# Performance work log

Measured on AMD Instinct MI355X. Metric: run time of the kernel, lower is better.

Reference implementation:

```python
import jax, jax.numpy as jnp
import numpy as np

BATCH, NUM_MASKS, IN_DIM, OUT_DIM = 512, 16, 1024, 1024


def setup_inputs() -> dict:
    key = jax.random.key(0)
    k1, k2, k3 = jax.random.split(key, 3)
    x = jax.random.normal(k1, (BATCH, NUM_MASKS, IN_DIM), dtype=jnp.float32)
    kernel = jax.random.normal(k2, (IN_DIM, OUT_DIM), dtype=jnp.float32) * (1.0 / np.sqrt(IN_DIM))
    masks = jax.random.uniform(k3, (NUM_MASKS, IN_DIM, OUT_DIM), dtype=jnp.float32)
    return {"x": x, "kernel": kernel, "masks": masks}


def reference(x, kernel, masks):
    # masked_kernel[m, i, o] = kernel[i, o] * masks[m, i, o]
    masked_kernel = kernel[None, :, :] * masks  # (M, I, O)
    # Original tf.scan serializes batch; equivalent math is one batched einsum:
    # out[b, m, o] = sum_i x[b, m, i] * masked_kernel[m, i, o]
    # NOTE: the executed tf.scan path applies NO activation, so neither do we.
    out = jnp.einsum('bmi,mio->bmo', x, masked_kernel)  # (B, M, O)
    return out
```

## Files before the change

kernel.cpp:

```cpp
#include <hip/hip_runtime.h>
#include <hip/hip_bf16.h>


#define BATCH 512
#define NMASK 16
#define IN_D  1024
#define OUT_D 1024

#define BM 128
#define BN 128
#define BK 32
#define NT (IN_D / BK)
#define AKP 40
#define BKP 34
#define THREADS 512

using bf16x8 = __attribute__((ext_vector_type(8))) __bf16;
using bf16x4 = __attribute__((ext_vector_type(4))) __bf16;
using f32x4  = __attribute__((ext_vector_type(4))) float;
using f32x2  = __attribute__((ext_vector_type(2))) float;

typedef const __attribute__((address_space(1))) void gvoid_t;
typedef __attribute__((address_space(3))) void lvoid_t;

__device__ __forceinline__ void dma16(const void* g, const void* l) {
    __builtin_amdgcn_global_load_lds((gvoid_t*)(uintptr_t)g,
                                     (lvoid_t*)(uintptr_t)l, 16, 0, 0);
}

__global__ void __launch_bounds__(THREADS, 4)
mdl_mfma_kernel(const float* __restrict__ X,
                const float* __restrict__ Kn,
                const float* __restrict__ Mk,
                float* __restrict__ Out)
{
    __shared__ __align__(16) float          Mf[2][BK * BN];
    __shared__ __align__(16) unsigned short As[2][BM * AKP];
    __shared__ __align__(16) unsigned short Bs[2][BN * BKP];

    const int t = threadIdx.x;
    const int l = t & 63;
    const int w = t >> 6;

    const int raw = blockIdx.x;
    const int wg  = (raw & 7) * 64 + (raw >> 3);
    const int m   = wg >> 5;
    const int ob  = (wg >> 2) & 7;
    const int bb  = wg & 3;

    const int wr = w >> 2;
    const int wc = w & 3;

    f32x4 acc[4][2];
#pragma unroll
    for (int mi = 0; mi < 4; ++mi)
#pragma unroll
        for (int ni = 0; ni < 2; ++ni)
            acc[mi][ni] = (f32x4){0.f, 0.f, 0.f, 0.f};

    const int a_row = t >> 2;
    const int a_kh  = (t & 3) * 8;
    const int o2 = (t & 63) * 2;
    const int k4 = w * 4;

    const int obase = ob * BN;
    const float* Xa  = X + ((size_t)(bb * BM + a_row) * NMASK + m) * IN_D + a_kh;
    const float* Knb = Kn + obase + o2;
    const float* Mkm = Mk + (size_t)m * IN_D * OUT_D;

    auto DMA = [&](int tile, int buf) {
        const int kt = tile * BK;
#pragma unroll
        for (int j = 0; j < 2; ++j) {
            const int k = j * 16 + w * 2 + (l >> 5);
            const float* gsrc = Mkm + (size_t)(kt + k) * OUT_D + obase + (l & 31) * 4;
            const float* ldst = &Mf[buf][j * 2048 + w * 256];
            dma16(gsrc, ldst);
        }
    };

    auto MFMA_PHASE = [&](int buf) {
        const int kg = (l >> 4) * 8;
        bf16x8 bfv[2];
#pragma unroll
        for (int ni = 0; ni < 2; ++ni) {
            const int n = wc * 32 + ni * 16 + (l & 15);
            bf16x4 lo = *(const bf16x4*)(&Bs[buf][n * BKP + kg]);
            bf16x4 hi = *(const bf16x4*)(&Bs[buf][n * BKP + kg + 4]);
            bf16x8 f;
            f[0] = lo[0]; f[1] = lo[1]; f[2] = lo[2]; f[3] = lo[3];
            f[4] = hi[0]; f[5] = hi[1]; f[6] = hi[2]; f[7] = hi[3];
            bfv[ni] = f;
        }
#pragma unroll
        for (int mi = 0; mi < 4; ++mi) {
            const int r = wr * 64 + mi * 16 + (l & 15);
            bf16x8 af = *(const bf16x8*)(&As[buf][r * AKP + kg]);
#pragma unroll
            for (int ni = 0; ni < 2; ++ni)
                acc[mi][ni] = __builtin_amdgcn_mfma_f32_16x16x32_bf16(
                    af, bfv[ni], acc[mi][ni], 0, 0, 0);
        }
    };

    DMA(0, 0);
    asm volatile("s_waitcnt vmcnt(0)" ::: "memory");
    __builtin_amdgcn_s_barrier();
    __builtin_amdgcn_sched_barrier(0);

    for (int tt = 0; tt < NT; ++tt) {
        const int cur = tt & 1;
        const int kt  = tt * BK;

        f32x4 xv0 = *(const f32x4*)(Xa + kt);
        f32x4 xv1 = *(const f32x4*)(Xa + kt + 4);
        f32x2 kv[4];
#pragma unroll
        for (int r = 0; r < 4; ++r)
            kv[r] = *(const f32x2*)(Knb + (size_t)(kt + k4 + r) * OUT_D);
        __builtin_amdgcn_sched_barrier(0);

        if (tt + 1 < NT) DMA(tt + 1, cur ^ 1);
        __builtin_amdgcn_sched_barrier(0);

        {
            f32x2 mvv[4];
#pragma unroll
            for (int r = 0; r < 4; ++r)
                mvv[r] = *(const f32x2*)(&Mf[cur][(k4 + r) * BN + o2]);
#pragma unroll
            for (int c = 0; c < 2; ++c) {
                bf16x4 v;
#pragma unroll
                for (int r = 0; r < 4; ++r)
                    v[r] = (__bf16)(kv[r][c] * mvv[r][c]);
                *(bf16x4*)(&Bs[cur][(o2 + c) * BKP + k4]) = v;
            }
            bf16x8 va;
#pragma unroll
            for (int j = 0; j < 4; ++j) {
                va[j]     = (__bf16)xv0[j];
                va[4 + j] = (__bf16)xv1[j];
            }
            *(bf16x8*)(&As[cur][a_row * AKP + a_kh]) = va;
        }

        asm volatile("s_waitcnt lgkmcnt(0)" ::: "memory");
        __builtin_amdgcn_sched_barrier(0);
        __builtin_amdgcn_s_barrier();
        __builtin_amdgcn_sched_barrier(0);

        MFMA_PHASE(cur);

        asm volatile("s_waitcnt vmcnt(0)" ::: "memory");
        __builtin_amdgcn_sched_barrier(0);
        __builtin_amdgcn_s_barrier();
        __builtin_amdgcn_sched_barrier(0);
    }

    const int r0 = bb * BM + wr * 64 + (l >> 4) * 4;
    const int c0 = ob * BN + wc * 32 + (l & 15);
#pragma unroll
    for (int mi = 0; mi < 4; ++mi) {
#pragma unroll
        for (int j = 0; j < 4; ++j) {
            const size_t row = (size_t)(r0 + mi * 16 + j);
            float* op = Out + (row * NMASK + m) * OUT_D + c0;
#pragma unroll
            for (int ni = 0; ni < 2; ++ni)
                op[ni * 16] = acc[mi][ni][j];
        }
    }
}

extern "C" void kernel_launch(void* const* d_in, const int* in_sizes, int n_in,
                              void* d_out, int out_size, void* d_ws, size_t ws_size,
                              hipStream_t stream) {
    (void)in_sizes; (void)n_in; (void)d_ws; (void)ws_size; (void)out_size;
    const float* X  = (const float*)d_in[0];
    const float* Kn = (const float*)d_in[1];
    const float* Mk = (const float*)d_in[2];
    float* Out = (float*)d_out;

    const int nblocks = (BATCH / BM) * (OUT_D / BN) * NMASK;
    mdl_mfma_kernel<<<nblocks, THREADS, 0, stream>>>(X, Kn, Mk, Out);
}
```

Before: 52.19 us.

## Triple-buffer mask DMA with two-tile prefetch and single-buffer bf16 tiles

New measurement: 52.45 us. About the same (+0.5%).

```diff
diff --git a/kernel.cpp b/kernel.cpp
--- a/kernel.cpp
+++ b/kernel.cpp
@@ -13,6 +13,7 @@
 #define NT (IN_D / BK)
 #define AKP 40
 #define BKP 34
+#define MFSZ (BK * BN)
 #define THREADS 512
 
 using bf16x8 = __attribute__((ext_vector_type(8))) __bf16;
@@ -34,9 +35,9 @@
                 const float* __restrict__ Mk,
                 float* __restrict__ Out)
 {
-    __shared__ __align__(16) float          Mf[2][BK * BN];
-    __shared__ __align__(16) unsigned short As[2][BM * AKP];
-    __shared__ __align__(16) unsigned short Bs[2][BN * BKP];
+    __shared__ __align__(16) float          Mf[3 * MFSZ];
+    __shared__ __align__(16) unsigned short As[BM * AKP];
+    __shared__ __align__(16) unsigned short Bs[BN * BKP];
 
     const int t = threadIdx.x;
     const int l = t & 63;
@@ -68,25 +69,25 @@
     const float* Knb = Kn + obase + o2;
     const float* Mkm = Mk + (size_t)m * IN_D * OUT_D;
 
-    auto DMA = [&](int tile, int buf) {
+    auto DMA = [&](int tile, int c) {
         const int kt = tile * BK;
 #pragma unroll
         for (int j = 0; j < 2; ++j) {
             const int k = j * 16 + w * 2 + (l >> 5);
             const float* gsrc = Mkm + (size_t)(kt + k) * OUT_D + obase + (l & 31) * 4;
-            const float* ldst = &Mf[buf][j * 2048 + w * 256];
+            const float* ldst = &Mf[c * MFSZ + j * 2048 + w * 256];
             dma16(gsrc, ldst);
         }
     };
 
-    auto MFMA_PHASE = [&](int buf) {
+    auto MFMA_PHASE = [&]() {
         const int kg = (l >> 4) * 8;
         bf16x8 bfv[2];
 #pragma unroll
         for (int ni = 0; ni < 2; ++ni) {
             const int n = wc * 32 + ni * 16 + (l & 15);
-            bf16x4 lo = *(const bf16x4*)(&Bs[buf][n * BKP + kg]);
-            bf16x4 hi = *(const bf16x4*)(&Bs[buf][n * BKP + kg + 4]);
+            bf16x4 lo = *(const bf16x4*)(&Bs[n * BKP + kg]);
+            bf16x4 hi = *(const bf16x4*)(&Bs[n * BKP + kg + 4]);
             bf16x8 f;
             f[0] = lo[0]; f[1] = lo[1]; f[2] = lo[2]; f[3] = lo[3];
             f[4] = hi[0]; f[5] = hi[1]; f[6] = hi[2]; f[7] = hi[3];
@@ -95,7 +96,7 @@
 #pragma unroll
         for (int mi = 0; mi < 4; ++mi) {
             const int r = wr * 64 + mi * 16 + (l & 15);
-            bf16x8 af = *(const bf16x8*)(&As[buf][r * AKP + kg]);
+            bf16x8 af = *(const bf16x8*)(&As[r * AKP + kg]);
 #pragma unroll
             for (int ni = 0; ni < 2; ++ni)
                 acc[mi][ni] = __builtin_amdgcn_mfma_f32_16x16x32_bf16(
@@ -104,13 +105,16 @@
     };
 
     DMA(0, 0);
-    asm volatile("s_waitcnt vmcnt(0)" ::: "memory");
+    DMA(1, 1);
+    asm volatile("s_waitcnt vmcnt(2)" ::: "memory");
+    __builtin_amdgcn_sched_barrier(0);
     __builtin_amdgcn_s_barrier();
     __builtin_amdgcn_sched_barrier(0);
 
+    int c_cur = 0, c_nxt = 1, c_far = 2;
+
     for (int tt = 0; tt < NT; ++tt) {
-        const int cur = tt & 1;
-        const int kt  = tt * BK;
+        const int kt = tt * BK;
 
         f32x4 xv0 = *(const f32x4*)(Xa + kt);
         f32x4 xv1 = *(const f32x4*)(Xa + kt + 4);
@@ -120,21 +124,22 @@
             kv[r] = *(const f32x2*)(Knb + (size_t)(kt + k4 + r) * OUT_D);
         __builtin_amdgcn_sched_barrier(0);
 
-        if (tt + 1 < NT) DMA(tt + 1, cur ^ 1);
+        const int tile_pf = (tt + 2 < NT) ? (tt + 2) : 0;
+        DMA(tile_pf, c_far);
         __builtin_amdgcn_sched_barrier(0);
 
         {
             f32x2 mvv[4];
 #pragma unroll
             for (int r = 0; r < 4; ++r)
-                mvv[r] = *(const f32x2*)(&Mf[cur][(k4 + r) * BN + o2]);
+                mvv[r] = *(const f32x2*)(&Mf[c_cur * MFSZ + (k4 + r) * BN + o2]);
 #pragma unroll
             for (int c = 0; c < 2; ++c) {
                 bf16x4 v;
 #pragma unroll
                 for (int r = 0; r < 4; ++r)
                     v[r] = (__bf16)(kv[r][c] * mvv[r][c]);
-                *(bf16x4*)(&Bs[cur][(o2 + c) * BKP + k4]) = v;
+                *(bf16x4*)(&Bs[(o2 + c) * BKP + k4]) = v;
             }
             bf16x8 va;
 #pragma unroll
@@ -142,7 +147,7 @@
                 va[j]     = (__bf16)xv0[j];
                 va[4 + j] = (__bf16)xv1[j];
             }
-            *(bf16x8*)(&As[cur][a_row * AKP + a_kh]) = va;
+            *(bf16x8*)(&As[a_row * AKP + a_kh]) = va;
         }
 
         asm volatile("s_waitcnt lgkmcnt(0)" ::: "memory");
@@ -150,13 +155,19 @@
         __builtin_amdgcn_s_barrier();
         __builtin_amdgcn_sched_barrier(0);
 
-        MFMA_PHASE(cur);
+        __builtin_amdgcn_s_setprio(1);
+        MFMA_PHASE();
+        __builtin_amdgcn_s_setprio(0);
 
-        asm volatile("s_waitcnt vmcnt(0)" ::: "memory");
+        asm volatile("s_waitcnt vmcnt(2)" ::: "memory");
         __builtin_amdgcn_sched_barrier(0);
         __builtin_amdgcn_s_barrier();
         __builtin_amdgcn_sched_barrier(0);
+
+        const int tmp = c_cur; c_cur = c_nxt; c_nxt = c_far; c_far = tmp;
     }
+
+    asm volatile("s_waitcnt vmcnt(0)" ::: "memory");
 
     const int r0 = bb * BM + wr * 64 + (l >> 4) * 4;
     const int c0 = ob * BN + wc * 32 + (l & 15);
```
